# Kernel optimization log

Hardware: AMD Instinct MI355X
Metric: run time of the kernel (lower is better)

Reference implementation:

```python
import jax, jax.numpy as jnp
import numpy as np

IN_DIM, IN_CAPS, OUT_CAPS, OUT_DIM = 8, 1152, 10, 16
NUM_ROUTING = 3
BATCH = 512


def squash(x, dim=-1):
    # NOTE: faithful to the source, which computes the squash factors but
    # then returns x unchanged (bug in original: `return x`).
    return x


def setup_inputs() -> dict:
    key = jax.random.key(0)
    k1, k2 = jax.random.split(key)
    x = jax.random.normal(k1, (BATCH, IN_CAPS, IN_DIM), dtype=jnp.float32)
    W = 0.01 * jax.random.normal(k2, (1, OUT_CAPS, IN_CAPS, OUT_DIM, IN_DIM), dtype=jnp.float32)
    return {"x": x, "W": W}


def reference(x, W):
    # u_hat[b,o,c,d] = sum_i W[0,o,c,d,i] * x[b,c,i]
    u_hat = jnp.einsum('ocdi,bci->bocd', W[0], x)  # [B, out_caps, in_caps, out_dim]
    temp_u_hat = jax.lax.stop_gradient(u_hat)
    B = x.shape[0]
    b = jnp.zeros((B, OUT_CAPS, IN_CAPS, 1), dtype=u_hat.dtype)

    def route_step(b, _):
        c = jax.nn.softmax(b, axis=1)                   # [B, O, C, 1]
        s = jnp.sum(c * temp_u_hat, axis=2)             # [B, O, D]
        v = squash(s)                                   # identity (source bug)
        uv = jnp.einsum('bocd,bod->boc', temp_u_hat, v)[..., None]
        return b + uv, None

    b, _ = jax.lax.scan(route_step, b, None, length=NUM_ROUTING - 1)
    c = jax.nn.softmax(b, axis=1)
    s = jnp.sum(c * u_hat, axis=2)                      # [B, O, D]
    v = squash(s)
    return v
```

## Files before the change

kernel.cpp:

```cpp
#include <hip/hip_runtime.h>
#include <hip/hip_bf16.h>

#define IN_DIM   8
#define IN_CAPS  1152
#define OUT_CAPS 10
#define OUT_DIM  16
#define BATCH    512
#define CSPLIT   24
#define CCHUNK   (IN_CAPS / CSPLIT)
#define NT4      (CCHUNK / 4)
#define BT       16
#define NBT      (BATCH / BT)
#define SSZ      (BATCH * OUT_CAPS * OUT_DIM)
#define SROW     164
#define ACCROW   168
#define ACCWAVE  (16 * ACCROW)

typedef float  f32x4 __attribute__((ext_vector_type(4)));
typedef short  s16x8 __attribute__((ext_vector_type(8)));

static __device__ __forceinline__ short f2bs(float f) {
  __hip_bfloat16 h = __float2bfloat16(f);
  short s;
  __builtin_memcpy(&s, &h, 2);
  return s;
}

template<int MODE>
__global__ __launch_bounds__(256, 3) void sweep_kernel(
    const float* __restrict__ x, const float* __restrict__ W,
    const float* __restrict__ sA, const float* __restrict__ sB,
    float* __restrict__ sOut) {
  __shared__ short s_bf[16 * SROW];
  __shared__ float sacc[4 * ACCWAVE];

  const int tid  = threadIdx.x;
  const int wid  = tid >> 6;
  const int lane = tid & 63;
  const int b    = lane & 15;
  const int g    = lane >> 4;
  const int bt   = blockIdx.x / CSPLIT;
  const int ch   = blockIdx.x % CSPLIT;
  const int c0   = ch * CCHUNK;
  const int bb0  = bt * BT;

  if (MODE != 0) {
    for (int k = tid; k < 16 * 160; k += 256) {
      int bb = k / 160, od = k % 160;
      float v = sA[(size_t)(bb0 + bb) * 160 + od];
      if (MODE == 2) v += sB[(size_t)(bb0 + bb) * 160 + od];
      s_bf[bb * SROW + od] = f2bs(v);
    }
  }
  for (int k = tid; k < 4 * ACCWAVE; k += 256) sacc[k] = 0.f;
  __syncthreads();

  f32x4 acc[OUT_CAPS];
  #pragma unroll
  for (int o = 0; o < OUT_CAPS; ++o) acc[o] = (f32x4){0.f, 0.f, 0.f, 0.f};

  const int isub = 4 * (g & 1);

  for (int t = wid; t < NT4; t += 4) {
    const int c4 = c0 + t * 4;
    const int cA = c4 + (g >> 1);
    const int cB = c4 + 2 + (g >> 1);
    const float4 xq0 = *(const float4*)(x + ((size_t)(bb0 + b) * IN_CAPS + cA) * IN_DIM + isub);
    const float4 xq1 = *(const float4*)(x + ((size_t)(bb0 + b) * IN_CAPS + cB) * IN_DIM + isub);

    float lg[2][OUT_CAPS];

    if (MODE != 0) {
      #pragma unroll
      for (int o = 0; o < OUT_CAPS; ++o) {
        ushort4 sv = *(const ushort4*)&s_bf[b * SROW + o * 16 + 4 * g];
        s16x8 sb = {(short)sv.x, (short)sv.y, (short)sv.z, (short)sv.w, 0, 0, 0, 0};
        #pragma unroll
        for (int h = 0; h < 2; ++h) {
          const int cm = c4 + 2 * h + (b >> 3);
          const float* wp = W + (((size_t)o * IN_CAPS + cm) * OUT_DIM + 4 * g) * IN_DIM + (b & 7);
          s16x8 a1 = {f2bs(wp[0]), f2bs(wp[8]), f2bs(wp[16]), f2bs(wp[24]), 0, 0, 0, 0};
          f32x4 zz = (f32x4){0.f, 0.f, 0.f, 0.f};
          f32x4 d1 = __builtin_amdgcn_mfma_f32_16x16x32_bf16(a1, sb, zz, 0, 0, 0);
          const float4 xq = h ? xq1 : xq0;
          float p = d1[0] * xq.x + d1[1] * xq.y + d1[2] * xq.z + d1[3] * xq.w;
          p += __shfl_xor(p, 16);
          lg[h][o] = p;
        }
      }
      #pragma unroll
      for (int h = 0; h < 2; ++h) {
        float m = lg[h][0];
        #pragma unroll
        for (int o = 1; o < OUT_CAPS; ++o) m = fmaxf(m, lg[h][o]);
        float sum = 0.f;
        #pragma unroll
        for (int o = 0; o < OUT_CAPS; ++o) { lg[h][o] = __expf(lg[h][o] - m); sum += lg[h][o]; }
        float inv = 1.f / sum;
        #pragma unroll
        for (int o = 0; o < OUT_CAPS; ++o) lg[h][o] *= inv;
      }
    }

    #pragma unroll
    for (int o = 0; o < OUT_CAPS; ++o) {
      const float cwA = (MODE == 0) ? 0.1f : lg[0][o];
      const float cwB = (MODE == 0) ? 0.1f : lg[1][o];
      s16x8 z8 = {f2bs(cwA * xq0.x), f2bs(cwA * xq0.y), f2bs(cwA * xq0.z), f2bs(cwA * xq0.w),
                  f2bs(cwB * xq1.x), f2bs(cwB * xq1.y), f2bs(cwB * xq1.z), f2bs(cwB * xq1.w)};
      const float4 wva = *(const float4*)(W + (((size_t)o * IN_CAPS + cA) * OUT_DIM + b) * IN_DIM + isub);
      const float4 wvb = *(const float4*)(W + (((size_t)o * IN_CAPS + cB) * OUT_DIM + b) * IN_DIM + isub);
      s16x8 a2 = {f2bs(wva.x), f2bs(wva.y), f2bs(wva.z), f2bs(wva.w),
                  f2bs(wvb.x), f2bs(wvb.y), f2bs(wvb.z), f2bs(wvb.w)};
      acc[o] = __builtin_amdgcn_mfma_f32_16x16x32_bf16(a2, z8, acc[o], 0, 0, 0);
    }
  }

  {
    float* sa = &sacc[wid * ACCWAVE + b * ACCROW];
    #pragma unroll
    for (int o = 0; o < OUT_CAPS; ++o) {
      #pragma unroll
      for (int r = 0; r < 4; ++r) sa[o * 16 + 4 * g + r] = acc[o][r];
    }
  }
  __syncthreads();

  for (int k = tid; k < 16 * 160; k += 256) {
    int bb = k / 160, od = k % 160;
    float v = sacc[0 * ACCWAVE + bb * ACCROW + od] + sacc[1 * ACCWAVE + bb * ACCROW + od] +
              sacc[2 * ACCWAVE + bb * ACCROW + od] + sacc[3 * ACCWAVE + bb * ACCROW + od];
    atomicAdd(&sOut[(size_t)(bb0 + bb) * 160 + od], v);
  }
}

extern "C" void kernel_launch(void* const* d_in, const int* in_sizes, int n_in,
                              void* d_out, int out_size, void* d_ws, size_t ws_size,
                              hipStream_t stream) {
  const float* x = (const float*)d_in[0];
  const float* W = (const float*)d_in[1];
  float* out = (float*)d_out;
  float* wsA = (float*)d_ws;
  float* wsB = wsA + SSZ;
  const size_t SB = (size_t)SSZ * sizeof(float);
  const int GRID = NBT * CSPLIT;

  hipMemsetAsync(d_ws, 0, 2 * SB, stream);
  sweep_kernel<0><<<GRID, 256, 0, stream>>>(x, W, wsA, wsB, wsA);
  sweep_kernel<1><<<GRID, 256, 0, stream>>>(x, W, wsA, wsB, wsB);
  sweep_kernel<2><<<GRID, 256, 0, stream>>>(x, W, wsA, wsB, out);
}
```

Before: 201.9 us.

## Replace global atomics with per-chunk partials and reduce kernel, stage x in LDS

```diff
diff --git a/kernel.cpp b/kernel.cpp
--- a/kernel.cpp
+++ b/kernel.cpp
@@ -6,7 +6,7 @@
 #define OUT_CAPS 10
 #define OUT_DIM  16
 #define BATCH    512
-#define CSPLIT   24
+#define CSPLIT   32
 #define CCHUNK   (IN_CAPS / CSPLIT)
 #define NT4      (CCHUNK / 4)
 #define BT       16
@@ -14,7 +14,8 @@
 #define SSZ      (BATCH * OUT_CAPS * OUT_DIM)
 #define SROW     164
 #define ACCROW   168
-#define ACCWAVE  (16 * ACCROW)
+#define XROW     (CCHUNK * IN_DIM + 4)
+#define PARTSZ   (CSPLIT * SSZ)
 
 typedef float  f32x4 __attribute__((ext_vector_type(4)));
 typedef short  s16x8 __attribute__((ext_vector_type(8)));
@@ -27,12 +28,13 @@
 }
 
 template<int MODE>
-__global__ __launch_bounds__(256, 3) void sweep_kernel(
+__global__ __launch_bounds__(256, 4) void sweep_kernel(
     const float* __restrict__ x, const float* __restrict__ W,
     const float* __restrict__ sA, const float* __restrict__ sB,
-    float* __restrict__ sOut) {
+    float* __restrict__ part) {
   __shared__ short s_bf[16 * SROW];
-  __shared__ float sacc[4 * ACCWAVE];
+  __shared__ float xs[16 * XROW];
+  __shared__ float sacc[16 * ACCROW];
 
   const int tid  = threadIdx.x;
   const int wid  = tid >> 6;
@@ -44,6 +46,11 @@
   const int c0   = ch * CCHUNK;
   const int bb0  = bt * BT;
 
+  for (int idx = tid; idx < 16 * 72; idx += 256) {
+    int bb = idx / 72, j = idx % 72;
+    *(float4*)(xs + bb * XROW + j * 4) =
+        *(const float4*)(x + ((size_t)(bb0 + bb) * IN_CAPS + c0) * IN_DIM + j * 4);
+  }
   if (MODE != 0) {
     for (int k = tid; k < 16 * 160; k += 256) {
       int bb = k / 160, od = k % 160;
@@ -52,7 +59,7 @@
       s_bf[bb * SROW + od] = f2bs(v);
     }
   }
-  for (int k = tid; k < 4 * ACCWAVE; k += 256) sacc[k] = 0.f;
+  for (int k = tid; k < 16 * ACCROW; k += 256) sacc[k] = 0.f;
   __syncthreads();
 
   f32x4 acc[OUT_CAPS];
@@ -62,11 +69,12 @@
   const int isub = 4 * (g & 1);
 
   for (int t = wid; t < NT4; t += 4) {
-    const int c4 = c0 + t * 4;
-    const int cA = c4 + (g >> 1);
-    const int cB = c4 + 2 + (g >> 1);
-    const float4 xq0 = *(const float4*)(x + ((size_t)(bb0 + b) * IN_CAPS + cA) * IN_DIM + isub);
-    const float4 xq1 = *(const float4*)(x + ((size_t)(bb0 + b) * IN_CAPS + cB) * IN_DIM + isub);
+    const int clA = t * 4 + (g >> 1);
+    const int clB = clA + 2;
+    const int cA  = c0 + clA;
+    const int cB  = c0 + clB;
+    const float4 xq0 = *(const float4*)(xs + b * XROW + clA * IN_DIM + isub);
+    const float4 xq1 = *(const float4*)(xs + b * XROW + clB * IN_DIM + isub);
 
     float lg[2][OUT_CAPS];
 
@@ -77,7 +85,7 @@
         s16x8 sb = {(short)sv.x, (short)sv.y, (short)sv.z, (short)sv.w, 0, 0, 0, 0};
         #pragma unroll
         for (int h = 0; h < 2; ++h) {
-          const int cm = c4 + 2 * h + (b >> 3);
+          const int cm = c0 + t * 4 + 2 * h + (b >> 3);
           const float* wp = W + (((size_t)o * IN_CAPS + cm) * OUT_DIM + 4 * g) * IN_DIM + (b & 7);
           s16x8 a1 = {f2bs(wp[0]), f2bs(wp[8]), f2bs(wp[16]), f2bs(wp[24]), 0, 0, 0, 0};
           f32x4 zz = (f32x4){0.f, 0.f, 0.f, 0.f};
@@ -117,21 +125,35 @@
   }
 
   {
-    float* sa = &sacc[wid * ACCWAVE + b * ACCROW];
+    float* sa = &sacc[b * ACCROW];
     #pragma unroll
     for (int o = 0; o < OUT_CAPS; ++o) {
       #pragma unroll
-      for (int r = 0; r < 4; ++r) sa[o * 16 + 4 * g + r] = acc[o][r];
+      for (int r = 0; r < 4; ++r) atomicAdd(&sa[o * 16 + 4 * g + r], acc[o][r]);
     }
   }
   __syncthreads();
 
-  for (int k = tid; k < 16 * 160; k += 256) {
-    int bb = k / 160, od = k % 160;
-    float v = sacc[0 * ACCWAVE + bb * ACCROW + od] + sacc[1 * ACCWAVE + bb * ACCROW + od] +
-              sacc[2 * ACCWAVE + bb * ACCROW + od] + sacc[3 * ACCWAVE + bb * ACCROW + od];
-    atomicAdd(&sOut[(size_t)(bb0 + bb) * 160 + od], v);
+  {
+    float4* dst = (float4*)(part + ((size_t)ch * BATCH + bb0) * 160);
+    for (int k = tid; k < 640; k += 256) {
+      int bb = k / 40, q = k % 40;
+      dst[k] = *(const float4*)(sacc + bb * ACCROW + q * 4);
+    }
   }
+}
+
+__global__ __launch_bounds__(256) void reduce_kernel(
+    const float* __restrict__ part, float* __restrict__ dst) {
+  const int i = blockIdx.x * 256 + threadIdx.x;
+  const float4* p4 = (const float4*)part;
+  float4 s = p4[i];
+  #pragma unroll
+  for (int ch = 1; ch < CSPLIT; ++ch) {
+    float4 a = p4[(size_t)ch * (SSZ / 4) + i];
+    s.x += a.x; s.y += a.y; s.z += a.z; s.w += a.w;
+  }
+  ((float4*)dst)[i] = s;
 }
 
 extern "C" void kernel_launch(void* const* d_in, const int* in_sizes, int n_in,
@@ -139,14 +161,16 @@
                               hipStream_t stream) {
   const float* x = (const float*)d_in[0];
   const float* W = (const float*)d_in[1];
-  float* out = (float*)d_out;
-  float* wsA = (float*)d_ws;
-  float* wsB = wsA + SSZ;
-  const size_t SB = (size_t)SSZ * sizeof(float);
+  float* out  = (float*)d_out;
+  float* part = (float*)d_ws;
+  float* wsA  = part + PARTSZ;
+  float* wsB  = wsA + SSZ;
   const int GRID = NBT * CSPLIT;
 
-  hipMemsetAsync(d_ws, 0, 2 * SB, stream);
-  sweep_kernel<0><<<GRID, 256, 0, stream>>>(x, W, wsA, wsB, wsA);
-  sweep_kernel<1><<<GRID, 256, 0, stream>>>(x, W, wsA, wsB, wsB);
-  sweep_kernel<2><<<GRID, 256, 0, stream>>>(x, W, wsA, wsB, out);
+  sweep_kernel<0><<<GRID, 256, 0, stream>>>(x, W, wsA, wsB, part);
+  reduce_kernel<<<SSZ / 4 / 256, 256, 0, stream>>>(part, wsA);
+  sweep_kernel<1><<<GRID, 256, 0, stream>>>(x, W, wsA, wsB, part);
+  reduce_kernel<<<SSZ / 4 / 256, 256, 0, stream>>>(part, wsB);
+  sweep_kernel<2><<<GRID, 256, 0, stream>>>(x, W, wsA, wsB, part);
+  reduce_kernel<<<SSZ / 4 / 256, 256, 0, stream>>>(part, out);
 }
```

New measurement: 306.1 us. +51.6%, slower.
